# Performance work log

Measured on AMD Instinct MI355X. Metric: run time of the kernel, lower is better.

## Reference

```python
import jax, jax.numpy as jnp
import numpy as np

EPS = 1e-5
SLOPE = 0.01  # LeakyReLU default negative_slope
D_STATE = 16


def leaky(x):
    return jnp.where(x >= 0, x, SLOPE * x)


def instance_norm(x):
    # InstanceNorm3d(affine=False): normalize per (n, c) over spatial dims
    m = x.mean(axis=(2, 3, 4), keepdims=True)
    v = x.var(axis=(2, 3, 4), keepdims=True)
    return (x - m) * jax.lax.rsqrt(v + EPS)


def conv3d(x, w, b, groups=1, pad=0):
    y = jax.lax.conv_general_dilated(
        x, w, (1, 1, 1), [(pad, pad)] * 3,
        dimension_numbers=('NCDHW', 'OIDHW', 'NCDHW'),
        feature_group_count=groups)
    return y + b[None, :, None, None, None]


def conv_transpose2(x, w, b):
    # ConvTranspose3d(k=2, s=2): non-overlapping, so it is a pure einsum+interleave
    # x: [n,c,d,h,w], w: [c,o,2,2,2] (torch layout)
    y = jnp.einsum('ncdhw,coijk->nodihjwk', x, w)
    n, o, d, _, h, _, ww, _ = y.shape
    return y.reshape(n, o, 2 * d, 2 * h, 2 * ww) + b[None, :, None, None, None]


def selective_scan(u, dt, A, B, C, D):
    # u, dt: [b,l,d]; A: [d,n]; B, C: [b,l,n]; D: [d]
    dA = jnp.exp(dt[..., None] * A)                              # [b,l,d,n]
    dBu = dt[..., None] * B[:, :, None, :] * u[..., None]        # [b,l,d,n]

    def step(h, inp):
        dA_t, dBu_t, C_t = inp
        h = dA_t * h + dBu_t                                     # [b,d,n]
        y = jnp.einsum('bdn,bn->bd', h, C_t)
        return h, y

    h0 = jnp.zeros((u.shape[0],) + A.shape, u.dtype)
    _, ys = jax.lax.scan(
        step, h0,
        (dA.transpose(1, 0, 2, 3), dBu.transpose(1, 0, 2, 3), C.transpose(1, 0, 2)))
    return ys.transpose(1, 0, 2) + u * D                         # [b,l,d]


def mamba_block(x, in_proj_w, conv1d_w, conv1d_b, x_proj_w,
                dt_proj_w, dt_proj_b, A_log, D_param, out_proj_w):
    # x: [b,l,c]
    dt_rank = dt_proj_w.shape[1]
    xz = x @ in_proj_w.T                                         # [b,l,2*d_inner]
    xi, z = jnp.split(xz, 2, axis=-1)
    # causal depthwise conv1d over sequence (torch pads d_conv-1 both sides, keeps [:L])
    xi_c = xi.transpose(0, 2, 1)                                 # [b,d_inner,l]
    xi_c = jax.lax.conv_general_dilated(
        xi_c, conv1d_w, (1,), [(conv1d_w.shape[-1] - 1, 0)],
        dimension_numbers=('NCH', 'OIH', 'NCH'),
        feature_group_count=xi_c.shape[1])
    xi = jax.nn.silu(xi_c + conv1d_b[None, :, None]).transpose(0, 2, 1)  # [b,l,d_inner]
    x_dbl = xi @ x_proj_w.T
    dt, B, C = jnp.split(x_dbl, [dt_rank, dt_rank + D_STATE], axis=-1)
    dt = jax.nn.softplus(dt @ dt_proj_w.T + dt_proj_b)
    A = -jnp.exp(A_log)
    y = selective_scan(xi, dt, A, B, C, D_param)
    y = y * jax.nn.silu(z)
    return y @ out_proj_w.T


def layer_norm(x, w, b):
    m = x.mean(-1, keepdims=True)
    v = x.var(-1, keepdims=True)
    return (x - m) * jax.lax.rsqrt(v + EPS) * w + b


def up_forward(x1, x2, up_w, up_b, dc1_w, dc1_b, dc2_w, dc2_b, dc3_w, dc3_b,
               ln_w, ln_b, in_proj_w, conv1d_w, conv1d_b, x_proj_w,
               dt_proj_w, dt_proj_b, A_log, D_param, out_proj_w):
    x1 = conv_transpose2(x1, up_w, up_b)
    dZ = x2.shape[2] - x1.shape[2]
    dY = x2.shape[3] - x1.shape[3]
    dX = x2.shape[4] - x1.shape[4]
    x1 = jnp.pad(x1, ((0, 0), (0, 0),
                      (dZ // 2, dZ - dZ // 2),
                      (dY // 2, dY - dY // 2),
                      (dX // 2, dX - dX // 2)))
    x = jnp.concatenate([x2, x1], axis=1)
    # DoubleConv (residual=False since in_channels != out_channels)
    x = leaky(instance_norm(conv3d(x, dc1_w, dc1_b)))
    x = leaky(instance_norm(conv3d(x, dc2_w, dc2_b, groups=8, pad=1)))
    x = leaky(instance_norm(conv3d(x, dc3_w, dc3_b)))
    # MambaLayer over flattened spatial tokens
    b, c, d, h, w = x.shape
    t = x.transpose(0, 2, 3, 4, 1).reshape(b, d * h * w, c)
    t = layer_norm(t, ln_w, ln_b)
    t = mamba_block(t, in_proj_w, conv1d_w, conv1d_b, x_proj_w,
                    dt_proj_w, dt_proj_b, A_log, D_param, out_proj_w)
    return t.reshape(b, d, h, w, c).transpose(0, 4, 1, 2, 3)


def setup_inputs() -> dict:
    key = jax.random.key(0)
    ks = jax.random.split(key, 20)
    c_out = 32      # out_channels / d_model
    d_inner = 64    # expand * d_model
    dt_rank = 2     # ceil(32/16)
    s = 0.02
    return {
        'x1': jax.random.normal(ks[0], (2, 32, 8, 16, 16), jnp.float32),
        'x2': jax.random.normal(ks[1], (2, 32, 16, 32, 32), jnp.float32),
        'up_w': jax.random.normal(ks[2], (32, 32, 2, 2, 2), jnp.float32) * s,
        'up_b': jnp.zeros((32,), jnp.float32),
        'dc1_w': jax.random.normal(ks[3], (32, 64, 1, 1, 1), jnp.float32) * s,
        'dc1_b': jnp.zeros((32,), jnp.float32),
        'dc2_w': jax.random.normal(ks[4], (32, 4, 3, 3, 3), jnp.float32) * s,
        'dc2_b': jnp.zeros((32,), jnp.float32),
        'dc3_w': jax.random.normal(ks[5], (32, 32, 1, 1, 1), jnp.float32) * s,
        'dc3_b': jnp.zeros((32,), jnp.float32),
        'ln_w': jnp.ones((c_out,), jnp.float32),
        'ln_b': jnp.zeros((c_out,), jnp.float32),
        'in_proj_w': jax.random.normal(ks[6], (2 * d_inner, c_out), jnp.float32) * s,
        'conv1d_w': jax.random.normal(ks[7], (d_inner, 1, 4), jnp.float32) * s,
        'conv1d_b': jnp.zeros((d_inner,), jnp.float32),
        'x_proj_w': jax.random.normal(ks[8], (dt_rank + 2 * D_STATE, d_inner), jnp.float32) * s,
        'dt_proj_w': jax.random.normal(ks[9], (d_inner, dt_rank), jnp.float32) * s,
        'dt_proj_b': jnp.full((d_inner,), -4.0, jnp.float32),
        'A_log': jnp.log(jnp.tile(jnp.arange(1.0, D_STATE + 1.0, dtype=jnp.float32), (d_inner, 1))),
        'D_param': jnp.ones((d_inner,), jnp.float32),
        'out_proj_w': jax.random.normal(ks[10], (c_out, d_inner), jnp.float32) * s,
    }


def reference(x1, x2, up_w, up_b, dc1_w, dc1_b, dc2_w, dc2_b, dc3_w, dc3_b,
              ln_w, ln_b, in_proj_w, conv1d_w, conv1d_b, x_proj_w,
              dt_proj_w, dt_proj_b, A_log, D_param, out_proj_w):
    return up_forward(x1, x2, up_w, up_b, dc1_w, dc1_b, dc2_w, dc2_b, dc3_w, dc3_b,
                      ln_w, ln_b, in_proj_w, conv1d_w, conv1d_b, x_proj_w,
                      dt_proj_w, dt_proj_b, A_log, D_param, out_proj_w)
```

## Files before the change

kernel.cpp:

```cpp
#include <hip/hip_runtime.h>

#define TPB 256
#define S_TOT 16384
#define NCHUNK 256
#define EPS 1e-5f
#define SLOPE 0.01f

__device__ __forceinline__ float leakyf(float v){ return v > 0.f ? v : SLOPE * v; }
__device__ __forceinline__ float siluf(float v){ return v / (1.f + __expf(-v)); }

__global__ __launch_bounds__(TPB) void k_upc1(
    const float* __restrict__ x1, const float* __restrict__ x2,
    const float* __restrict__ upw, const float* __restrict__ upb,
    const float* __restrict__ w1, const float* __restrict__ b1,
    float* __restrict__ c1, float* st1p) {
  __shared__ float wq[8192];
  __shared__ float sup[64*33];
  __shared__ float red[4][8][2];
  int t = threadIdx.x, bid = blockIdx.x;
  int sb = bid & 255, n = bid >> 8;
  int p = t & 63, os = t >> 6;
  int s = sb*64 + p;
  for (int i = t; i < 8192; i += TPB) wq[i] = upw[i];
  __syncthreads();
  int z = s >> 10, y = (s >> 5) & 31, x = s & 31;
  int tap = ((z & 1)*2 + (y & 1))*2 + (x & 1);
  int xb = n*65536 + (z >> 1)*256 + (y >> 1)*16 + (x >> 1);
  float xv[32];
  #pragma unroll
  for (int c = 0; c < 32; c++) xv[c] = x1[xb + c*2048];
  float up[8];
  #pragma unroll
  for (int j = 0; j < 8; j++) up[j] = upb[os*8 + j];
  #pragma unroll
  for (int c = 0; c < 32; c++) {
    #pragma unroll
    for (int j = 0; j < 8; j++)
      up[j] += xv[c] * wq[c*256 + (os*8 + j)*8 + tap];
  }
  #pragma unroll
  for (int j = 0; j < 8; j++) sup[p*33 + os*8 + j] = up[j];
  __syncthreads();
  int c0 = os*8;
  float acc[8];
  #pragma unroll
  for (int j = 0; j < 8; j++) acc[j] = b1[c0 + j];
  const float* px2 = x2 + n*32*S_TOT + s;
  #pragma unroll
  for (int i = 0; i < 32; i++) {
    float v = px2[i*S_TOT];
    #pragma unroll
    for (int j = 0; j < 8; j++) acc[j] += v * w1[(c0 + j)*64 + i];
  }
  #pragma unroll
  for (int o = 0; o < 32; o++) {
    float v = sup[p*33 + o];
    #pragma unroll
    for (int j = 0; j < 8; j++) acc[j] += v * w1[(c0 + j)*64 + 32 + o];
  }
  #pragma unroll
  for (int j = 0; j < 8; j++)
    c1[(n*32 + c0 + j)*S_TOT + s] = acc[j];
  int wv = t >> 6;
  #pragma unroll
  for (int j = 0; j < 8; j++) {
    float sm = acc[j], sq = acc[j]*acc[j];
    #pragma unroll
    for (int o = 32; o > 0; o >>= 1) { sm += __shfl_down(sm, o); sq += __shfl_down(sq, o); }
    if ((t & 63) == 0) { red[wv][j][0] = sm; red[wv][j][1] = sq; }
  }
  __syncthreads();
  if (t < 64) {
    int w2 = t >> 4, j = (t >> 1) & 7, m = t & 1;
    st1p[((n*32 + w2*8 + j)*2 + m)*256 + sb] = red[w2][j][m];
  }
}

__global__ __launch_bounds__(TPB) void k_conv2(
    const float* __restrict__ c1, const float* __restrict__ w,
    const float* __restrict__ bias, const float* st1p,
    float* __restrict__ c2, float* st2p) {
  __shared__ float ws[432];
  __shared__ float tile[4080];
  __shared__ float smom[4][2];
  __shared__ float mrs[4][2];
  __shared__ float red[4][4][2];
  int bid = blockIdx.x, t = threadIdx.x;
  int sb = bid & 63, g = (bid >> 6) & 7, n = bid >> 9;
  int s0 = sb << 8;
  int z = s0 >> 10, y0 = (s0 >> 5) & 31;
  for (int i = t; i < 432; i += TPB) ws[i] = w[g*432 + i];
  {
    int pp = t >> 5, l = t & 31;
    if (pp < 8) {
      int j = pp & 3, m = pp >> 2;
      const float* sp = st1p + ((n*32 + g*4 + j)*2 + m)*256;
      float v = 0.f;
      #pragma unroll
      for (int k = 0; k < 8; k++) v += sp[l + 32*k];
      v += __shfl_down(v, 16); v += __shfl_down(v, 8); v += __shfl_down(v, 4);
      v += __shfl_down(v, 2);  v += __shfl_down(v, 1);
      if (l == 0) smom[j][m] = v;
    }
  }
  __syncthreads();
  if (t < 4) {
    float m = smom[t][0] * (1.f/S_TOT);
    mrs[t][0] = m; mrs[t][1] = rsqrtf(smom[t][1]*(1.f/S_TOT) - m*m + EPS);
  }
  __syncthreads();
  const float* cbase = c1 + (n*32 + g*4)*S_TOT;
  for (int i = t; i < 4080; i += TPB) {
    int ic = i / 1020, r = i - ic*1020;
    int zo = r / 340, r2 = r - zo*340;
    int yo = r2 / 34, xo = r2 - yo*34;
    int zz = z + zo - 1, yy = y0 + yo - 1, xx = xo - 1;
    float v = 0.f;
    if (zz >= 0 && zz < 16 && yy >= 0 && yy < 32 && xx >= 0 && xx < 32)
      v = leakyf((cbase[ic*S_TOT + zz*1024 + yy*32 + xx] - mrs[ic][0]) * mrs[ic][1]);
    tile[i] = v;
  }
  __syncthreads();
  int ty = t >> 5, x = t & 31;
  int s = s0 + t;
  float acc[4];
  #pragma unroll
  for (int oc = 0; oc < 4; oc++) acc[oc] = bias[g*4 + oc];
  #pragma unroll
  for (int ic = 0; ic < 4; ic++) {
    #pragma unroll
    for (int dz = 0; dz < 3; dz++) {
      #pragma unroll
      for (int dy = 0; dy < 3; dy++) {
        const float* tr = tile + ((ic*3 + dz)*10 + ty + dy)*34 + x;
        float p0 = tr[0], p1 = tr[1], p2 = tr[2];
        int wb = ic*27 + dz*9 + dy*3;
        #pragma unroll
        for (int oc = 0; oc < 4; oc++) {
          const float* wo = &ws[oc*108 + wb];
          acc[oc] += p0*wo[0] + p1*wo[1] + p2*wo[2];
        }
      }
    }
  }
  float sm[4], sq[4];
  #pragma unroll
  for (int oc = 0; oc < 4; oc++) {
    c2[(n*32 + g*4 + oc)*S_TOT + s] = acc[oc];
    sm[oc] = acc[oc]; sq[oc] = acc[oc]*acc[oc];
  }
  #pragma unroll
  for (int o = 32; o > 0; o >>= 1) {
    #pragma unroll
    for (int oc = 0; oc < 4; oc++) {
      sm[oc] += __shfl_down(sm[oc], o);
      sq[oc] += __shfl_down(sq[oc], o);
    }
  }
  int lane = t & 63, wv = t >> 6;
  if (lane == 0) {
    #pragma unroll
    for (int oc = 0; oc < 4; oc++) { red[wv][oc][0] = sm[oc]; red[wv][oc][1] = sq[oc]; }
  }
  __syncthreads();
  if (t < 8) {
    int oc = t & 3, m = t >> 2;
    float a = red[0][oc][m] + red[1][oc][m] + red[2][oc][m] + red[3][oc][m];
    st2p[((n*32 + g*4 + oc)*2 + m)*64 + sb] = a;
  }
}

__global__ __launch_bounds__(TPB) void k_conv3(
    const float* __restrict__ c2, const float* __restrict__ w,
    const float* __restrict__ bias, const float* st2p,
    float* __restrict__ c3, float* st3p) {
  __shared__ float ws[256];
  __shared__ float ssum[32][2];
  __shared__ float mrs[32][2];
  __shared__ float red[4][8][2];
  int t = threadIdx.x;
  int idx = blockIdx.x * TPB + t;
  int s = idx & 16383;
  int n = (idx >> 14) & 1;
  int q = idx >> 15;
  int sb = blockIdx.x & 63;
  int c0 = q*8;
  if (t < 256) ws[t] = w[c0*32 + t];
  if (t < 64) {
    int c = t >> 1, m = t & 1;
    const float* sp = st2p + ((n*32 + c)*2 + m)*64;
    float v = 0.f;
    #pragma unroll
    for (int k = 0; k < 64; k++) v += sp[k];
    ssum[c][m] = v;
  }
  __syncthreads();
  if (t < 32) {
    float m = ssum[t][0] * (1.f/S_TOT);
    mrs[t][0] = m; mrs[t][1] = rsqrtf(ssum[t][1]*(1.f/S_TOT) - m*m + EPS);
  }
  __syncthreads();
  const float* pin = c2 + n*32*S_TOT + s;
  float acc[8];
  #pragma unroll
  for (int j = 0; j < 8; j++) acc[j] = bias[c0 + j];
  #pragma unroll
  for (int i = 0; i < 32; i++) {
    float v = leakyf((pin[i*S_TOT] - mrs[i][0]) * mrs[i][1]);
    #pragma unroll
    for (int j = 0; j < 8; j++) acc[j] += v * ws[j*32 + i];
  }
  #pragma unroll
  for (int j = 0; j < 8; j++)
    c3[(n*32 + c0 + j)*S_TOT + s] = acc[j];
  int wv = t >> 6;
  #pragma unroll
  for (int j = 0; j < 8; j++) {
    float sm = acc[j], sq = acc[j]*acc[j];
    #pragma unroll
    for (int o = 32; o > 0; o >>= 1) { sm += __shfl_down(sm, o); sq += __shfl_down(sq, o); }
    if ((t & 63) == 0) { red[wv][j][0] = sm; red[wv][j][1] = sq; }
  }
  __syncthreads();
  if (t < 16) {
    int j = t >> 1, m = t & 1;
    float a = red[0][j][m] + red[1][j][m] + red[2][j][m] + red[3][j][m];
    st3p[((n*32 + c0 + j)*2 + m)*64 + sb] = a;
  }
}

__global__ __launch_bounds__(TPB) void k_token(
    const float* __restrict__ c3, const float* st3p,
    const float* __restrict__ lnw, const float* __restrict__ lnb,
    const float* __restrict__ ipw, const float* __restrict__ c1w,
    const float* __restrict__ c1b, const float* __restrict__ xpw,
    const float* __restrict__ dtw, const float* __restrict__ dtbi,
    float* __restrict__ zb, float* __restrict__ u, float* __restrict__ dt,
    float* __restrict__ Bb, float* __restrict__ Cc) {
  __shared__ float un[4224];
  __shared__ float xpf[3264];
  __shared__ float sxi[2240];
  __shared__ float lnwb[64];
  __shared__ float mrs[64];
  __shared__ float ssum[64];
  float* Wraw = un;
  float* tk   = un;
  float* mv   = un + 1280;
  float* su2  = un;
  float* xd   = un + 2176;

  int t = threadIdx.x, bid = blockIdx.x;
  int tok0 = bid * 32;
  int n = tok0 >> 14, s0 = tok0 & 16383;

  if (t < 64) {
    int c = t >> 1, m = t & 1;
    const float* sp = st3p + ((n*32 + c)*2 + m)*64;
    float v = 0.f;
    #pragma unroll
    for (int k = 0; k < 64; k++) v += sp[k];
    ssum[c*2 + m] = v;
  }
  for (int i = t; i < 4096; i += TPB) {
    int f = i >> 5, c = i & 31;
    Wraw[f*33 + c] = ipw[i];
  }
  for (int i = t; i < 3264; i += TPB) {
    int f = i / 68, dd = i - f*68;
    xpf[i] = (f < 34 && dd < 64) ? xpw[f*64 + dd] : 0.f;
  }
  if (t < 32) { lnwb[t] = lnw[t]; lnwb[32 + t] = lnb[t]; }
  __syncthreads();
  if (t < 32) {
    float m = ssum[t*2] * (1.f/S_TOT);
    mrs[t*2] = m; mrs[t*2 + 1] = rsqrtf(ssum[t*2 + 1]*(1.f/S_TOT) - m*m + EPS);
  }
  int fr = t & 127, half = t >> 7;
  float wreg[32];
  float S1 = 0.f, S2 = 0.f;
  #pragma unroll
  for (int c = 0; c < 32; c++) {
    float wa = Wraw[fr*33 + c];
    wreg[c] = wa * lnwb[c];
    S1 += wreg[c];
    S2 += wa * lnwb[32 + c];
  }
  __syncthreads();
  for (int i = t; i < 1120; i += TPB) {
    int c = i / 35, lt = i - c*35;
    int sg = s0 - 3 + lt;
    int sgc = sg < 0 ? 0 : sg;
    float raw = c3[(n*32 + c)*S_TOT + sgc];
    tk[lt*36 + c] = leakyf((raw - mrs[c*2]) * mrs[c*2 + 1]);
  }
  __syncthreads();
  if (t < 35) {
    float mean = 0.f;
    #pragma unroll
    for (int c = 0; c < 32; c++) mean += tk[t*36 + c];
    mean *= (1.f/32.f);
    float var = 0.f;
    #pragma unroll
    for (int c = 0; c < 32; c++) { float d2 = tk[t*36 + c] - mean; var += d2*d2; }
    mv[t*2] = mean; mv[t*2 + 1] = rsqrtf(var*(1.f/32.f) + EPS);
  }
  __syncthreads();
  for (int lt = half; lt < 35; lt += 2) {
    float acc = 0.f;
    #pragma unroll
    for (int c4 = 0; c4 < 8; c4++) {
      float4 tq = *(const float4*)(tk + lt*36 + 4*c4);
      acc += wreg[4*c4]*tq.x + wreg[4*c4+1]*tq.y + wreg[4*c4+2]*tq.z + wreg[4*c4+3]*tq.w;
    }
    float mean = mv[lt*2], rst = mv[lt*2 + 1];
    float r = rst*(acc - mean*S1) + S2;
    int sg = s0 - 3 + lt;
    if (fr < 64) {
      sxi[lt*64 + fr] = (sg < 0) ? 0.f : r;
    } else if (lt >= 3) {
      zb[(tok0 + lt - 3)*64 + (fr - 64)] = r;
    }
  }
  __syncthreads();
  int ch = t & 63;
  {
    float cw0 = c1w[ch*4], cw1 = c1w[ch*4+1], cw2 = c1w[ch*4+2], cw3 = c1w[ch*4+3];
    float cb = c1b[ch];
    #pragma unroll
    for (int r = 0; r < 8; r++) {
      int lt = (t >> 6) + 4*r;
      float acc = cb + sxi[lt*64 + ch]*cw0 + sxi[(lt+1)*64 + ch]*cw1
                     + sxi[(lt+2)*64 + ch]*cw2 + sxi[(lt+3)*64 + ch]*cw3;
      float uv = siluf(acc);
      u[(tok0 + lt)*64 + ch] = uv;
      su2[lt*68 + ch] = uv;
    }
  }
  __syncthreads();
  #pragma unroll
  for (int pass = 0; pass < 2; pass++) {
    int lt = (t >> 4) + pass*16;
    int f0 = (t & 15)*3;
    const float* sr = su2 + lt*68;
    const float* xr0 = xpf + f0*68;
    const float* xr1 = xpf + (f0+1)*68;
    const float* xr2 = xpf + (f0+2)*68;
    float a0 = 0.f, a1 = 0.f, a2 = 0.f;
    #pragma unroll
    for (int c4 = 0; c4 < 16; c4++) {
      float4 uq = *(const float4*)(sr + 4*c4);
      float4 q0 = *(const float4*)(xr0 + 4*c4);
      float4 q1 = *(const float4*)(xr1 + 4*c4);
      float4 q2 = *(const float4*)(xr2 + 4*c4);
      a0 += uq.x*q0.x + uq.y*q0.y + uq.z*q0.z + uq.w*q0.w;
      a1 += uq.x*q1.x + uq.y*q1.y + uq.z*q1.z + uq.w*q1.w;
      a2 += uq.x*q2.x + uq.y*q2.y + uq.z*q2.z + uq.w*q2.w;
    }
    if (f0     < 34) xd[lt*34 + f0]     = a0;
    if (f0 + 1 < 34) xd[lt*34 + f0 + 1] = a1;
    if (f0 + 2 < 34) xd[lt*34 + f0 + 2] = a2;
  }
  __syncthreads();
  {
    float dw0 = dtw[ch*2], dw1 = dtw[ch*2+1], db = dtbi[ch];
    #pragma unroll
    for (int r = 0; r < 8; r++) {
      int lt = (t >> 6) + 4*r;
      int token = tok0 + lt;
      float dv = xd[lt*34]*dw0 + xd[lt*34 + 1]*dw1 + db;
      dt[token*64 + ch] = fmaxf(dv, 0.f) + log1pf(__expf(-fabsf(dv)));
      if (ch < 16)      Bb[token*16 + ch]      = xd[lt*34 + 2 + ch];
      else if (ch < 32) Cc[token*16 + ch - 16] = xd[lt*34 + 2 + ch];
    }
  }
}


__global__ __launch_bounds__(TPB) void k_scan1(
    const float* __restrict__ dt, const float* __restrict__ u,
    const float* __restrict__ Bb, const float* __restrict__ Alog,
    float* __restrict__ cA, float* __restrict__ cX) {
  __shared__ __align__(16) float sdt[1024], su[1024], sB[256];
  int bid = blockIdx.x, t = threadIdx.x;
  int chunk = bid & 255, b = bid >> 8;
  int q = t & 3, d = t >> 2;
  float Ar[4];
  #pragma unroll
  for (int j = 0; j < 4; j++) Ar[j] = -__expf(Alog[d*16 + 4*q + j]);
  float h[4] = {0.f,0.f,0.f,0.f};
  float sdts = 0.f;
  int tg0 = b*S_TOT + chunk*64;
  for (int tile = 0; tile < 4; tile++) {
    int base = tg0 + tile*16;
    {
      int i = t*4;
      *(float4*)(sdt + i) = *(const float4*)(dt + base*64 + i);
      *(float4*)(su  + i) = *(const float4*)(u  + base*64 + i);
    }
    sB[t] = Bb[base*16 + t];
    __syncthreads();
    #pragma unroll
    for (int tt = 0; tt < 16; tt++) {
      float dtv = sdt[tt*64 + d], uv = su[tt*64 + d];
      sdts += dtv;
      float du = dtv * uv;
      float4 Bq = *(const float4*)(sB + tt*16 + q*4);
      h[0] = __expf(Ar[0]*dtv)*h[0] + Bq.x*du;
      h[1] = __expf(Ar[1]*dtv)*h[1] + Bq.y*du;
      h[2] = __expf(Ar[2]*dtv)*h[2] + Bq.z*du;
      h[3] = __expf(Ar[3]*dtv)*h[3] + Bq.w*du;
    }
    __syncthreads();
  }
  #pragma unroll
  for (int j = 0; j < 4; j++) {
    int idx = (((b*64 + d)*16 + 4*q + j)*NCHUNK) + chunk;
    cA[idx] = __expf(Ar[j]*sdts);
    cX[idx] = h[j];
  }
}

__global__ __launch_bounds__(TPB) void k_scan2(
    const float* __restrict__ cA, float* __restrict__ cX) {
  int t = threadIdx.x;
  int w = blockIdx.x*4 + (t >> 6);
  int lane = t & 63;
  int b = w >> 10, d = (w >> 4) & 63, nn = w & 15;
  int base = ((b*64 + d)*16 + nn)*NCHUNK;
  float4 a = *(const float4*)(cA + base + lane*4);
  float4 x = *(const float4*)(cX + base + lane*4);
  float A = a.x*a.y*a.z*a.w;
  float X = ((x.x*a.y + x.y)*a.z + x.z)*a.w + x.w;
  #pragma unroll
  for (int off = 1; off < 64; off <<= 1) {
    float Ap = __shfl_up(A, off);
    float Xp = __shfl_up(X, off);
    if (lane >= off) { X = A*Xp + X; A = A*Ap; }
  }
  float Xe = __shfl_up(X, 1);
  if (lane == 0) Xe = 0.f;
  float r = Xe;
  float4 o;
  o.x = r; r = a.x*r + x.x;
  o.y = r; r = a.y*r + x.y;
  o.z = r; r = a.z*r + x.z;
  o.w = r;
  *(float4*)(cX + base + lane*4) = o;
}

__global__ __launch_bounds__(TPB) void k_scan3(
    const float* __restrict__ dt, const float* __restrict__ u,
    const float* __restrict__ Bb, const float* __restrict__ Cc,
    const float* __restrict__ Alog, const float* __restrict__ Dp,
    const float* __restrict__ zb, const float* __restrict__ cX,
    const float* __restrict__ opw, float* __restrict__ out) {
  __shared__ __align__(16) float sdt[1024], su[1024], sB[256], sC[256];
  __shared__ float gt[64*65];
  int bid = blockIdx.x, t = threadIdx.x;
  int chunk = bid & 255, b = bid >> 8;
  int q = t & 3, d = t >> 2;
  float Ar[4];
  #pragma unroll
  for (int j = 0; j < 4; j++) Ar[j] = -__expf(Alog[d*16 + 4*q + j]);
  float h[4];
  #pragma unroll
  for (int j = 0; j < 4; j++)
    h[j] = cX[(((b*64 + d)*16 + 4*q + j)*NCHUNK) + chunk];
  float Dv = Dp[d];
  int tg0 = b*S_TOT + chunk*64;
  for (int tile = 0; tile < 4; tile++) {
    int base = tg0 + tile*16;
    {
      int i = t*4;
      *(float4*)(sdt + i) = *(const float4*)(dt + base*64 + i);
      *(float4*)(su  + i) = *(const float4*)(u  + base*64 + i);
    }
    for (int i = t; i < 1024; i += TPB)
      gt[(tile*16 + (i >> 6))*65 + (i & 63)] = zb[base*64 + i];
    sB[t] = Bb[base*16 + t];
    sC[t] = Cc[base*16 + t];
    __syncthreads();
    #pragma unroll
    for (int tt = 0; tt < 16; tt++) {
      float dtv = sdt[tt*64 + d], uv = su[tt*64 + d];
      float du = dtv * uv;
      float4 Bq = *(const float4*)(sB + tt*16 + q*4);
      float4 Cq = *(const float4*)(sC + tt*16 + q*4);
      h[0] = __expf(Ar[0]*dtv)*h[0] + Bq.x*du;
      h[1] = __expf(Ar[1]*dtv)*h[1] + Bq.y*du;
      h[2] = __expf(Ar[2]*dtv)*h[2] + Bq.z*du;
      h[3] = __expf(Ar[3]*dtv)*h[3] + Bq.w*du;
      float yp = h[0]*Cq.x + h[1]*Cq.y + h[2]*Cq.z + h[3]*Cq.w;
      yp += __shfl_xor(yp, 1);
      yp += __shfl_xor(yp, 2);
      if (q == 0) {
        float zv = gt[(tile*16 + tt)*65 + d];
        gt[(tile*16 + tt)*65 + d] = (yp + uv*Dv) * siluf(zv);
      }
    }
    __syncthreads();
  }
  {
    int sl = t & 63, cb = t >> 6;
    float acc[8] = {0.f,0.f,0.f,0.f,0.f,0.f,0.f,0.f};
    const float* wp = opw + cb*8*64;
    #pragma unroll
    for (int dd = 0; dd < 64; dd++) {
      float v = gt[sl*65 + dd];
      #pragma unroll
      for (int j = 0; j < 8; j++) acc[j] += v * wp[j*64 + dd];
    }
    #pragma unroll
    for (int j = 0; j < 8; j++)
      out[(b*32 + cb*8 + j)*S_TOT + chunk*64 + sl] = acc[j];
  }
}

extern "C" void kernel_launch(void* const* d_in, const int* in_sizes, int n_in,
                              void* d_out, int out_size, void* d_ws, size_t ws_size,
                              hipStream_t stream) {
  const float* x1    = (const float*)d_in[0];
  const float* x2    = (const float*)d_in[1];
  const float* upw   = (const float*)d_in[2];
  const float* upb   = (const float*)d_in[3];
  const float* dc1w  = (const float*)d_in[4];
  const float* dc1b  = (const float*)d_in[5];
  const float* dc2w  = (const float*)d_in[6];
  const float* dc2b  = (const float*)d_in[7];
  const float* dc3w  = (const float*)d_in[8];
  const float* dc3b  = (const float*)d_in[9];
  const float* lnw   = (const float*)d_in[10];
  const float* lnb   = (const float*)d_in[11];
  const float* ipw   = (const float*)d_in[12];
  const float* c1w   = (const float*)d_in[13];
  const float* c1b   = (const float*)d_in[14];
  const float* xpw   = (const float*)d_in[15];
  const float* dtw   = (const float*)d_in[16];
  const float* dtbi  = (const float*)d_in[17];
  const float* Alog  = (const float*)d_in[18];
  const float* Dp    = (const float*)d_in[19];
  const float* opw   = (const float*)d_in[20];
  float* out = (float*)d_out;

  float* ws = (float*)d_ws;
  float* st1p  = ws + 0;
  float* st2p  = ws + 32768;
  float* st3p  = ws + 40960;
  float* c1    = ws + 49152;
  float* c2    = ws + 1097728;
  float* c3    = ws + 2146304;
  float* zb    = ws + 3194880;
  float* ub    = ws + 5292032;
  float* dtb   = ws + 7389184;
  float* Bb    = ws + 9486336;
  float* Cc    = ws + 10010624;
  float* cA    = ws + 10534912;
  float* cX    = ws + 11059200;

  k_upc1 <<<512,  TPB, 0, stream>>>(x1, x2, upw, upb, dc1w, dc1b, c1, st1p);
  k_conv2<<<1024, TPB, 0, stream>>>(c1, dc2w, dc2b, st1p, c2, st2p);
  k_conv3<<<512,  TPB, 0, stream>>>(c2, dc3w, dc3b, st2p, c3, st3p);
  k_token<<<1024, TPB, 0, stream>>>(c3, st3p, lnw, lnb, ipw, c1w, c1b, xpw,
                                    dtw, dtbi, zb, ub, dtb, Bb, Cc);
  k_scan1<<<512,  TPB, 0, stream>>>(dtb, ub, Bb, Alog, cA, cX);
  k_scan2<<<512,  TPB, 0, stream>>>(cA, cX);
  k_scan3<<<512,  TPB, 0, stream>>>(dtb, ub, Bb, Cc, Alog, Dp, zb, cX, opw, out);
}
```

Baseline: 237.3 us.

## Halve scan chunk length to double scan parallelism, vectorize stats reduction

Splits the selective scan into 512 chunks of 32 tokens instead of 256 chunks of 64, doubling the block count of the chunk-local scan and output kernels. The inter-chunk scan now processes 8 chunk carries per lane. The token kernel's per-channel stat reduction is spread over all threads with float4 loads and shuffles, and its small dot product uses four independent accumulators. This trades more carry traffic and a longer prefix step for better GPU occupancy in the scan passes.

```diff
diff --git a/kernel.cpp b/kernel.cpp
--- a/kernel.cpp
+++ b/kernel.cpp
@@ -2,7 +2,8 @@
 
 #define TPB 256
 #define S_TOT 16384
-#define NCHUNK 256
+#define NCHUNK 512
+#define CLEN 32
 #define EPS 1e-5f
 #define SLOPE 0.01f
 
@@ -253,13 +254,18 @@
   int tok0 = bid * 32;
   int n = tok0 >> 14, s0 = tok0 & 16383;
 
-  if (t < 64) {
-    int c = t >> 1, m = t & 1;
-    const float* sp = st3p + ((n*32 + c)*2 + m)*64;
-    float v = 0.f;
-    #pragma unroll
-    for (int k = 0; k < 64; k++) v += sp[k];
-    ssum[c*2 + m] = v;
+  {
+    int pair = t >> 2, k4 = t & 3;
+    const float* sp = st3p + (n*64 + pair)*64 + k4*16;
+    float4 v0 = *(const float4*)(sp);
+    float4 v1 = *(const float4*)(sp + 4);
+    float4 v2 = *(const float4*)(sp + 8);
+    float4 v3 = *(const float4*)(sp + 12);
+    float v = v0.x+v0.y+v0.z+v0.w + v1.x+v1.y+v1.z+v1.w
+            + v2.x+v2.y+v2.z+v2.w + v3.x+v3.y+v3.z+v3.w;
+    v += __shfl_xor(v, 1);
+    v += __shfl_xor(v, 2);
+    if (k4 == 0) ssum[pair] = v;
   }
   for (int i = t; i < 4096; i += TPB) {
     int f = i >> 5, c = i & 31;
@@ -306,12 +312,16 @@
   }
   __syncthreads();
   for (int lt = half; lt < 35; lt += 2) {
-    float acc = 0.f;
+    float a0 = 0.f, a1 = 0.f, a2 = 0.f, a3 = 0.f;
     #pragma unroll
     for (int c4 = 0; c4 < 8; c4++) {
       float4 tq = *(const float4*)(tk + lt*36 + 4*c4);
-      acc += wreg[4*c4]*tq.x + wreg[4*c4+1]*tq.y + wreg[4*c4+2]*tq.z + wreg[4*c4+3]*tq.w;
-    }
+      a0 += wreg[4*c4]*tq.x;
+      a1 += wreg[4*c4+1]*tq.y;
+      a2 += wreg[4*c4+2]*tq.z;
+      a3 += wreg[4*c4+3]*tq.w;
+    }
+    float acc = (a0 + a1) + (a2 + a3);
     float mean = mv[lt*2], rst = mv[lt*2 + 1];
     float r = rst*(acc - mean*S1) + S2;
     int sg = s0 - 3 + lt;
@@ -382,15 +392,15 @@
     float* __restrict__ cA, float* __restrict__ cX) {
   __shared__ __align__(16) float sdt[1024], su[1024], sB[256];
   int bid = blockIdx.x, t = threadIdx.x;
-  int chunk = bid & 255, b = bid >> 8;
+  int chunk = bid & (NCHUNK-1), b = bid >> 9;
   int q = t & 3, d = t >> 2;
   float Ar[4];
   #pragma unroll
   for (int j = 0; j < 4; j++) Ar[j] = -__expf(Alog[d*16 + 4*q + j]);
   float h[4] = {0.f,0.f,0.f,0.f};
   float sdts = 0.f;
-  int tg0 = b*S_TOT + chunk*64;
-  for (int tile = 0; tile < 4; tile++) {
+  int tg0 = b*S_TOT + chunk*CLEN;
+  for (int tile = 0; tile < 2; tile++) {
     int base = tg0 + tile*16;
     {
       int i = t*4;
@@ -427,10 +437,14 @@
   int lane = t & 63;
   int b = w >> 10, d = (w >> 4) & 63, nn = w & 15;
   int base = ((b*64 + d)*16 + nn)*NCHUNK;
-  float4 a = *(const float4*)(cA + base + lane*4);
-  float4 x = *(const float4*)(cX + base + lane*4);
-  float A = a.x*a.y*a.z*a.w;
-  float X = ((x.x*a.y + x.y)*a.z + x.z)*a.w + x.w;
+  float a[8], x[8];
+  *(float4*)(a)     = *(const float4*)(cA + base + lane*8);
+  *(float4*)(a + 4) = *(const float4*)(cA + base + lane*8 + 4);
+  *(float4*)(x)     = *(const float4*)(cX + base + lane*8);
+  *(float4*)(x + 4) = *(const float4*)(cX + base + lane*8 + 4);
+  float A = 1.f, X = 0.f;
+  #pragma unroll
+  for (int k = 0; k < 8; k++) { X = X*a[k] + x[k]; A *= a[k]; }
   #pragma unroll
   for (int off = 1; off < 64; off <<= 1) {
     float Ap = __shfl_up(A, off);
@@ -440,12 +454,11 @@
   float Xe = __shfl_up(X, 1);
   if (lane == 0) Xe = 0.f;
   float r = Xe;
-  float4 o;
-  o.x = r; r = a.x*r + x.x;
-  o.y = r; r = a.y*r + x.y;
-  o.z = r; r = a.z*r + x.z;
-  o.w = r;
-  *(float4*)(cX + base + lane*4) = o;
+  float o[8];
+  #pragma unroll
+  for (int k = 0; k < 8; k++) { o[k] = r; r = a[k]*r + x[k]; }
+  *(float4*)(cX + base + lane*8)     = *(float4*)(o);
+  *(float4*)(cX + base + lane*8 + 4) = *(float4*)(o + 4);
 }
 
 __global__ __launch_bounds__(TPB) void k_scan3(
@@ -455,9 +468,9 @@
     const float* __restrict__ zb, const float* __restrict__ cX,
     const float* __restrict__ opw, float* __restrict__ out) {
   __shared__ __align__(16) float sdt[1024], su[1024], sB[256], sC[256];
-  __shared__ float gt[64*65];
+  __shared__ float gt[32*65];
   int bid = blockIdx.x, t = threadIdx.x;
-  int chunk = bid & 255, b = bid >> 8;
+  int chunk = bid & (NCHUNK-1), b = bid >> 9;
   int q = t & 3, d = t >> 2;
   float Ar[4];
   #pragma unroll
@@ -467,8 +480,8 @@
   for (int j = 0; j < 4; j++)
     h[j] = cX[(((b*64 + d)*16 + 4*q + j)*NCHUNK) + chunk];
   float Dv = Dp[d];
-  int tg0 = b*S_TOT + chunk*64;
-  for (int tile = 0; tile < 4; tile++) {
+  int tg0 = b*S_TOT + chunk*CLEN;
+  for (int tile = 0; tile < 2; tile++) {
     int base = tg0 + tile*16;
     {
       int i = t*4;
@@ -501,18 +514,18 @@
     __syncthreads();
   }
   {
-    int sl = t & 63, cb = t >> 6;
-    float acc[8] = {0.f,0.f,0.f,0.f,0.f,0.f,0.f,0.f};
-    const float* wp = opw + cb*8*64;
+    int sl = t & 31, cb = t >> 5;
+    float acc[4] = {0.f,0.f,0.f,0.f};
+    const float* wp = opw + cb*4*64;
     #pragma unroll
     for (int dd = 0; dd < 64; dd++) {
       float v = gt[sl*65 + dd];
       #pragma unroll
-      for (int j = 0; j < 8; j++) acc[j] += v * wp[j*64 + dd];
-    }
-    #pragma unroll
-    for (int j = 0; j < 8; j++)
-      out[(b*32 + cb*8 + j)*S_TOT + chunk*64 + sl] = acc[j];
+      for (int j = 0; j < 4; j++) acc[j] += v * wp[j*64 + dd];
+    }
+    #pragma unroll
+    for (int j = 0; j < 4; j++)
+      out[(b*32 + cb*4 + j)*S_TOT + chunk*CLEN + sl] = acc[j];
   }
 }
 
@@ -555,14 +568,14 @@
   float* Bb    = ws + 9486336;
   float* Cc    = ws + 10010624;
   float* cA    = ws + 10534912;
-  float* cX    = ws + 11059200;
+  float* cX    = ws + 11583488;
 
   k_upc1 <<<512,  TPB, 0, stream>>>(x1, x2, upw, upb, dc1w, dc1b, c1, st1p);
   k_conv2<<<1024, TPB, 0, stream>>>(c1, dc2w, dc2b, st1p, c2, st2p);
   k_conv3<<<512,  TPB, 0, stream>>>(c2, dc3w, dc3b, st2p, c3, st3p);
   k_token<<<1024, TPB, 0, stream>>>(c3, st3p, lnw, lnb, ipw, c1w, c1b, xpw,
                                     dtw, dtbi, zb, ub, dtb, Bb, Cc);
-  k_scan1<<<512,  TPB, 0, stream>>>(dtb, ub, Bb, Alog, cA, cX);
+  k_scan1<<<1024, TPB, 0, stream>>>(dtb, ub, Bb, Alog, cA, cX);
   k_scan2<<<512,  TPB, 0, stream>>>(cA, cX);
-  k_scan3<<<512,  TPB, 0, stream>>>(dtb, ub, Bb, Cc, Alog, Dp, zb, cX, opw, out);
-}
+  k_scan3<<<1024, TPB, 0, stream>>>(dtb, ub, Bb, Cc, Alog, Dp, zb, cX, opw, out);
+}
```

After: 242.2 us. 1.02x slower.
